# Optimization experiments

Measured on AMD Instinct MI355X. Metric: run time of the kernel, lower is better.

## Reference

```python
import jax, jax.numpy as jnp
import numpy as np

WIN = 11  # hard-coded window size in the original module

def sinusoidal_pe(L, D):
    pos = jnp.arange(L, dtype=jnp.float32)[:, None]
    div = jnp.exp(jnp.arange(0, D, 2, dtype=jnp.float32) * (-np.log(10000.0) / D))
    pe = jnp.zeros((L, D), dtype=jnp.float32)
    pe = pe.at[:, 0::2].set(jnp.sin(pos * div))
    pe = pe.at[:, 1::2].set(jnp.cos(pos * div))
    return pe


def setup_inputs() -> dict:
    key = jax.random.key(0)
    ks = jax.random.split(key, 6)
    B, Lq, Ld, D, V = 16, 30, 1100, 768, 50000
    return {
        "q": jax.random.randint(ks[0], (B, Lq), 0, V),
        "d_pos": jax.random.randint(ks[1], (B, Ld), 0, V),
        "d_neg": jax.random.randint(ks[2], (B, Ld), 0, V),
        "q_mask": jnp.ones((B, Lq, 1), jnp.float32),
        "d_pos_mask": jnp.ones((B, Ld, 1), jnp.float32),
        "d_neg_mask": jnp.ones((B, Ld, 1), jnp.float32),
        "pe_flag": 1,
        "emb_table": jax.random.normal(ks[3], (V, D), jnp.float32) * 0.02,
        "W_lin": jax.random.normal(ks[4], (D, D), jnp.float32) * 0.02,
        "W_out": jax.random.normal(ks[5], (D, D), jnp.float32) * 0.02,
    }


def reference(q, d_pos, d_neg, q_mask, d_pos_mask, d_neg_mask, pe_flag, emb_table, W_lin, W_out):
    B, Lq = q.shape
    Ld = d_pos.shape[1]
    D = emb_table.shape[1]
    H = 12
    Dh = D // H
    W_num = Ld // WIN  # number of 11-token windows

    qe = emb_table[q] * q_mask              # [B,Lq,D]
    dp = emb_table[d_pos]                   # [B,Ld,D]
    dn = emb_table[d_neg]
    if pe_flag:
        pe = sinusoidal_pe(Ld, D)[None]     # [1,Ld,D]
        scale_emb = jnp.sqrt(jnp.float32(D))
        dp = dp * scale_emb + pe            # dropout p=0 -> identity
        dn = dn * scale_emb + pe
    dp = dp * d_pos_mask
    dn = dn * d_neg_mask

    dp = dp.reshape(B, W_num, WIN, D)       # [B,W,11,D]
    dn = dn.reshape(B, W_num, WIN, D)
    qx = jnp.broadcast_to(qe[:, None], (B, W_num, Lq, D))  # expand over windows

    # linear_trans (no bias): y = x @ W_lin.T
    queries = jnp.einsum('bwqd,ed->bwqe', qx, W_lin)
    dp = jnp.einsum('bwkd,ed->bwke', dp, W_lin)
    dn = jnp.einsum('bwkd,ed->bwke', dn, W_lin)

    # faithful replication of torch .view head-split: pure reshape, mixes seq+channel
    def split(x, L):
        return x.reshape(B, W_num, H, L, Dh)

    queries = split(queries, Lq) * (Dh ** -0.5)

    def attend(doc):
        d = split(doc, WIN)                                  # [B,W,H,11,Dh]
        logits = jnp.einsum('bwhqd,bwhkd->bwhqk', queries, d)
        weights = jax.nn.softmax(logits, axis=-1)            # dropout p=0
        ctx = jnp.einsum('bwhqk,bwhkd->bwhqd', weights, d)
        ctx = ctx.reshape(B, W_num, Lq, D)                   # faithful merge (.view)
        return jnp.einsum('bwqd,ed->bwqe', ctx, W_out)

    return attend(dp), attend(dn)
```

## Files before the change

kernel.cpp:

```cpp
#include <hip/hip_runtime.h>
#include <hip/hip_bf16.h>
#include <cstdint>
#include <cstddef>

#define B_    16
#define LQ    30
#define LD    1100
#define DIM   768
#define NH    12
#define DH_   64
#define WINSZ 11
#define WNUM  100
#define NSLOT 32

typedef __attribute__((ext_vector_type(8))) short short8;
typedef __attribute__((ext_vector_type(4))) float f32x4;

__device__ __forceinline__ void gload_lds16(const void* g, void* l) {
  __builtin_amdgcn_global_load_lds(
      (const __attribute__((address_space(1))) void*)g,
      (__attribute__((address_space(3))) void*)l, 16, 0, 0);
}

__global__ __launch_bounds__(256) void wconv_kernel(const float* __restrict__ wa,
    const float* __restrict__ wb, __hip_bfloat16* __restrict__ oa,
    __hip_bfloat16* __restrict__ ob) {
  int i = (blockIdx.x * 256 + threadIdx.x) * 4;
  if (i >= DIM * DIM) return;
  float4 va = *reinterpret_cast<const float4*>(wa + i);
  float4 vb = *reinterpret_cast<const float4*>(wb + i);
  union { __hip_bfloat16 h[4]; uint2 u; } pa, pb;
  pa.h[0] = __float2bfloat16(va.x); pa.h[1] = __float2bfloat16(va.y);
  pa.h[2] = __float2bfloat16(va.z); pa.h[3] = __float2bfloat16(va.w);
  pb.h[0] = __float2bfloat16(vb.x); pb.h[1] = __float2bfloat16(vb.y);
  pb.h[2] = __float2bfloat16(vb.z); pb.h[3] = __float2bfloat16(vb.w);
  *reinterpret_cast<uint2*>(oa + i) = pa.u;
  *reinterpret_cast<uint2*>(ob + i) = pb.u;
}

__global__ __launch_bounds__(256) void pe_kernel(float* __restrict__ pe) {
  int idx = blockIdx.x * 256 + threadIdx.x;
  if (idx >= LD * (DIM / 4)) return;
  int t  = idx / (DIM / 4);
  int c4 = idx % (DIM / 4);
  int i0 = c4 * 2;
  float d0 = expf(-0.023985261387f * (float)i0);
  float d1 = expf(-0.023985261387f * (float)(i0 + 1));
  float s0f, c0f, s1f, c1f;
  sincosf((float)t * d0, &s0f, &c0f);
  sincosf((float)t * d1, &s1f, &c1f);
  *reinterpret_cast<float4*>(pe + (size_t)t * DIM + c4 * 4) =
      make_float4(s0f, c0f, s1f, c1f);
}

__global__ __launch_bounds__(256) void prep_q_kernel(const int* __restrict__ q,
    const float* __restrict__ qmask, const float* __restrict__ emb,
    __hip_bfloat16* __restrict__ Xq) {
  int idx = blockIdx.x * 256 + threadIdx.x;
  if (idx >= B_ * LQ * (DIM / 4)) return;
  int row = idx / (DIM / 4);
  int c4  = idx % (DIM / 4);
  float m = qmask[row] * 0.125f;
  float4 v = *reinterpret_cast<const float4*>(emb + (size_t)q[row] * DIM + c4 * 4);
  union { __hip_bfloat16 h[4]; uint2 u; } o;
  o.h[0] = __float2bfloat16(v.x * m); o.h[1] = __float2bfloat16(v.y * m);
  o.h[2] = __float2bfloat16(v.z * m); o.h[3] = __float2bfloat16(v.w * m);
  *reinterpret_cast<uint2*>(Xq + (size_t)row * DIM + c4 * 4) = o.u;
}

__global__ __launch_bounds__(256) void prep_d_kernel(const int* __restrict__ dpos,
    const int* __restrict__ dneg, const float* __restrict__ dpmask,
    const float* __restrict__ dnmask, const float* __restrict__ emb,
    const int* __restrict__ peflag, const float* __restrict__ pe,
    __hip_bfloat16* __restrict__ X, int s0, int rows) {
  int idx = blockIdx.x * 256 + threadIdx.x;
  if (idx >= rows * (DIM / 4)) return;
  int r  = idx / (DIM / 4);
  int c4 = idx % (DIM / 4);
  int s = s0 + r / LD;
  int t = r % LD;
  int doc = s >> 4, b = s & 15;
  const int*   di = doc ? dneg   : dpos;
  const float* dm = doc ? dnmask : dpmask;
  int grow = b * LD + t;
  float m = dm[grow];
  float4 v = *reinterpret_cast<const float4*>(emb + (size_t)di[grow] * DIM + c4 * 4);
  if (peflag[0]) {
    float4 p = *reinterpret_cast<const float4*>(pe + (size_t)t * DIM + c4 * 4);
    v.x = v.x * 27.712812921102035f + p.x;
    v.y = v.y * 27.712812921102035f + p.y;
    v.z = v.z * 27.712812921102035f + p.z;
    v.w = v.w * 27.712812921102035f + p.w;
  }
  union { __hip_bfloat16 h[4]; uint2 u; } o;
  o.h[0] = __float2bfloat16(v.x * m); o.h[1] = __float2bfloat16(v.y * m);
  o.h[2] = __float2bfloat16(v.z * m); o.h[3] = __float2bfloat16(v.w * m);
  *reinterpret_cast<uint2*>(X + (size_t)r * DIM + c4 * 4) = o.u;
}

template <bool OUT_BF16>
__global__ __launch_bounds__(512, 2) void gemm_mfma(const __hip_bfloat16* __restrict__ A,
    const __hip_bfloat16* __restrict__ Bt, void* __restrict__ Cv,
    int M, int N, int K, int tilesX, int tiles1,
    const __hip_bfloat16* __restrict__ A2, float* __restrict__ C2, int M2) {
  extern __shared__ __hip_bfloat16 smem[];

  const int nwg  = gridDim.x;
  const int orig = blockIdx.x;
  const int q8 = nwg >> 3, r8 = nwg & 7;
  const int xcd = orig & 7, pos = orig >> 3;
  const int wgid = (xcd < r8 ? xcd * (q8 + 1) : r8 * (q8 + 1) + (xcd - r8) * q8) + pos;

  const bool is2 = (wgid >= tiles1);
  const int  w2  = is2 ? (wgid - tiles1) : wgid;
  const int row0 = (w2 / tilesX) * 256;
  const int col0 = (w2 % tilesX) * 256;
  const __hip_bfloat16* Ap = is2 ? A2 : A;
  const int Mloc = is2 ? M2 : M;

  const int tid  = threadIdx.x;
  const int lane = tid & 63;
  const int wave = tid >> 6;
  const int wr = wave >> 2, wc = wave & 3;
  const int lo4 = lane & 15;
  const int hi4 = lane >> 4;

  const int u0 = tid,        r0s = u0 >> 3, x0s = u0 & 7;
  const int u1 = 512 + tid,  r1s = u1 >> 3, x1s = u1 & 7;
  const int soff0 = r0s * K + ((x0s ^ (r0s & 7)) * 8);
  const int soff1 = r1s * K + ((x1s ^ (r1s & 7)) * 8);
  const int wvoff = wave * 512;
  const __hip_bfloat16* gA = Ap + (size_t)row0 * K;
  const __hip_bfloat16* gB = Bt + (size_t)col0 * K;

#define STAGE_HALF(PTR, KOFF, HALF, SLOTBASE)                            \
  gload_lds16((PTR) + (size_t)(HALF) * (128 * 768) + (KOFF) + soff0,    \
              smem + (SLOTBASE) + (HALF) * 8192 + wvoff);               \
  gload_lds16((PTR) + (size_t)(HALF) * (128 * 768) + (KOFF) + soff1,    \
              smem + (SLOTBASE) + (HALF) * 8192 + 4096 + wvoff);

  const int rA = (wr * 128 + lo4) * 64;
  const int rB = (wc * 64  + lo4) * 64;
  const int xk0 = ((0 + hi4) ^ (lo4 & 7)) * 8;
  const int xk1 = ((4 + hi4) ^ (lo4 & 7)) * 8;

#define LDA(S, MM, XK) (*reinterpret_cast<const short8*>(smem + (S) * 16384 + rA + (MM) * 1024 + (XK)))
#define LDB(S, NN, XK) (*reinterpret_cast<const short8*>(smem + 32768 + (S) * 16384 + rB + (NN) * 1024 + (XK)))

  f32x4 acc[8][4] = {};
  short8 bf[4][2];
  short8 xa0, xa1, xa2, xa3;
  short8 ya0, ya1, ya2, ya3;

#define MM4R(MMI, KK, AREG)                                                        \
  acc[MMI][0] = __builtin_amdgcn_mfma_f32_16x16x32_bf16(bf[0][KK], AREG, acc[MMI][0], 0, 0, 0); \
  acc[MMI][1] = __builtin_amdgcn_mfma_f32_16x16x32_bf16(bf[1][KK], AREG, acc[MMI][1], 0, 0, 0); \
  acc[MMI][2] = __builtin_amdgcn_mfma_f32_16x16x32_bf16(bf[2][KK], AREG, acc[MMI][2], 0, 0, 0); \
  acc[MMI][3] = __builtin_amdgcn_mfma_f32_16x16x32_bf16(bf[3][KK], AREG, acc[MMI][3], 0, 0, 0);
#define MFMA4R(MA, MB, R0, R1, R2, R3) \
  MM4R(MA, 0, R0) MM4R(MB, 0, R1) MM4R(MA, 1, R2) MM4R(MB, 1, R3)

#define LDB8(S)                                                          \
  bf[0][0] = LDB(S, 0, xk0); bf[1][0] = LDB(S, 1, xk0);                  \
  bf[2][0] = LDB(S, 2, xk0); bf[3][0] = LDB(S, 3, xk0);                  \
  bf[0][1] = LDB(S, 0, xk1); bf[1][1] = LDB(S, 1, xk1);                  \
  bf[2][1] = LDB(S, 2, xk1); bf[3][1] = LDB(S, 3, xk1);
#define LDA4R(S, MA, MB, R0, R1, R2, R3)                                 \
  R0 = LDA(S, MA, xk0); R1 = LDA(S, MB, xk0);                            \
  R2 = LDA(S, MA, xk1); R3 = LDA(S, MB, xk1);

#define BARR  { __builtin_amdgcn_s_barrier(); __builtin_amdgcn_sched_barrier(0); }
#define VMW(NLIT) asm volatile("s_waitcnt vmcnt(" NLIT ")" ::: "memory");
#define PH_SYNC(NLIT) { asm volatile("s_waitcnt lgkmcnt(" NLIT ")" ::: "memory"); \
                        __builtin_amdgcn_sched_barrier(0);               \
                        __builtin_amdgcn_s_setprio(1); }
#define PH_END  __builtin_amdgcn_s_setprio(0);

  STAGE_HALF(gB, 0,   0, 32768) STAGE_HALF(gB, 0,   1, 32768)
  STAGE_HALF(gA, 0,   0, 0)     STAGE_HALF(gA, 0,   1, 0)
  STAGE_HALF(gB, 64,  0, 49152) STAGE_HALF(gB, 64,  1, 49152)

  for (int it = 0; it < 5; ++it) {
    const int kb = it * 128;
    VMW("4") BARR
    LDB8(0)
    LDA4R(0, 0, 1, xa0, xa1, xa2, xa3)
    LDA4R(0, 2, 3, ya0, ya1, ya2, ya3)
    STAGE_HALF(gA, kb + 64, 0, 16384)
    PH_SYNC("4") MFMA4R(0, 1, xa0, xa1, xa2, xa3) PH_END
    BARR
    LDA4R(0, 4, 5, xa0, xa1, xa2, xa3)
    STAGE_HALF(gA, kb + 64, 1, 16384)
    PH_SYNC("4") MFMA4R(2, 3, ya0, ya1, ya2, ya3) PH_END
    BARR
    LDA4R(0, 6, 7, ya0, ya1, ya2, ya3)
    STAGE_HALF(gB, kb + 128, 0, 32768)
    PH_SYNC("4") MFMA4R(4, 5, xa0, xa1, xa2, xa3) PH_END
    BARR
    STAGE_HALF(gB, kb + 128, 1, 32768)
    PH_SYNC("0") MFMA4R(6, 7, ya0, ya1, ya2, ya3) PH_END
    VMW("4") BARR
    LDB8(1)
    LDA4R(1, 0, 1, xa0, xa1, xa2, xa3)
    LDA4R(1, 2, 3, ya0, ya1, ya2, ya3)
    STAGE_HALF(gA, kb + 128, 0, 0)
    PH_SYNC("4") MFMA4R(0, 1, xa0, xa1, xa2, xa3) PH_END
    BARR
    LDA4R(1, 4, 5, xa0, xa1, xa2, xa3)
    STAGE_HALF(gA, kb + 128, 1, 0)
    PH_SYNC("4") MFMA4R(2, 3, ya0, ya1, ya2, ya3) PH_END
    BARR
    LDA4R(1, 6, 7, ya0, ya1, ya2, ya3)
    STAGE_HALF(gB, kb + 192, 0, 49152)
    PH_SYNC("4") MFMA4R(4, 5, xa0, xa1, xa2, xa3) PH_END
    BARR
    STAGE_HALF(gB, kb + 192, 1, 49152)
    PH_SYNC("0") MFMA4R(6, 7, ya0, ya1, ya2, ya3) PH_END
  }

  VMW("4") BARR
  LDB8(0)
  LDA4R(0, 0, 1, xa0, xa1, xa2, xa3)
  LDA4R(0, 2, 3, ya0, ya1, ya2, ya3)
  STAGE_HALF(gA, 704, 0, 16384)
  PH_SYNC("4") MFMA4R(0, 1, xa0, xa1, xa2, xa3) PH_END
  BARR
  LDA4R(0, 4, 5, xa0, xa1, xa2, xa3)
  STAGE_HALF(gA, 704, 1, 16384)
  PH_SYNC("4") MFMA4R(2, 3, ya0, ya1, ya2, ya3) PH_END
  BARR
  LDA4R(0, 6, 7, ya0, ya1, ya2, ya3)
  PH_SYNC("4") MFMA4R(4, 5, xa0, xa1, xa2, xa3) PH_END
  BARR
  PH_SYNC("0") MFMA4R(6, 7, ya0, ya1, ya2, ya3) PH_END
  VMW("0") BARR
  LDB8(1)
  LDA4R(1, 0, 1, xa0, xa1, xa2, xa3)
  LDA4R(1, 2, 3, ya0, ya1, ya2, ya3)
  PH_SYNC("4") MFMA4R(0, 1, xa0, xa1, xa2, xa3) PH_END
  BARR
  LDA4R(1, 4, 5, xa0, xa1, xa2, xa3)
  PH_SYNC("4") MFMA4R(2, 3, ya0, ya1, ya2, ya3) PH_END
  BARR
  LDA4R(1, 6, 7, ya0, ya1, ya2, ya3)
  PH_SYNC("4") MFMA4R(4, 5, xa0, xa1, xa2, xa3) PH_END
  BARR
  PH_SYNC("0") MFMA4R(6, 7, ya0, ya1, ya2, ya3) PH_END

#undef STAGE_HALF
#undef LDA
#undef LDB
#undef MM4R
#undef MFMA4R
#undef LDB8
#undef LDA4R
#undef BARR
#undef VMW
#undef PH_SYNC
#undef PH_END

#pragma unroll
  for (int m = 0; m < 8; ++m) {
    const int r = row0 + wr * 128 + m * 16 + lo4;
    if (r < Mloc) {
#pragma unroll
      for (int n = 0; n < 4; ++n) {
        const int cb = col0 + wc * 64 + n * 16 + hi4 * 4;
        f32x4 v = acc[m][n];
        if (is2) {
          *reinterpret_cast<f32x4*>(C2 + (size_t)r * N + cb) = v;
        } else if constexpr (OUT_BF16) {
          union { __hip_bfloat16 h[4]; uint2 u; } p;
          p.h[0] = __float2bfloat16(v[0]); p.h[1] = __float2bfloat16(v[1]);
          p.h[2] = __float2bfloat16(v[2]); p.h[3] = __float2bfloat16(v[3]);
          *reinterpret_cast<uint2*>((__hip_bfloat16*)Cv + (size_t)r * N + cb) = p.u;
        } else {
          __builtin_nontemporal_store(
              v, reinterpret_cast<f32x4*>((float*)Cv + (size_t)r * N + cb));
        }
      }
    }
  }
}

__global__ __launch_bounds__(64) void attn_kernel(const float* __restrict__ Qs,
    const __hip_bfloat16* __restrict__ Y, __hip_bfloat16* __restrict__ ctx, int s0) {
  __shared__ alignas(16) __hip_bfloat16 Dk[16][80];
  __shared__ alignas(16) __hip_bfloat16 DlT[64][40];

  const int blk = blockIdx.x;
  const int w  = blk % WNUM;
  const int sl = blk / WNUM;
  const int b  = (s0 + sl) & 15;

  const int lane = threadIdx.x;
  const int lo4 = lane & 15, hi4 = lane >> 4;

  const __hip_bfloat16* Yw = Y + ((size_t)(sl * LD + w * WINSZ)) * DIM;
  const float* Qb = Qs + (size_t)(b * LQ) * DIM;
  __hip_bfloat16* cb = ctx + (size_t)(sl * WNUM + w) * (LQ * DIM);

  for (int h = 0; h < NH; ++h) {
    const uint4* src = reinterpret_cast<const uint4*>(Yw + h * (WINSZ * DH_));
    uint4 r0 = src[lane];
    uint4 r1 = (lane < 24) ? src[64 + lane] : make_uint4(0, 0, 0, 0);
    {
      int k = lane >> 3, d0 = (lane & 7) * 8;
      *reinterpret_cast<uint4*>(&Dk[k][d0]) = r0;
      const __hip_bfloat16* hp = reinterpret_cast<const __hip_bfloat16*>(&r0);
#pragma unroll
      for (int j = 0; j < 8; ++j) DlT[d0 + j][k] = hp[j];
    }
    if (lane < 24) {
      int i = 64 + lane;
      int k = i >> 3, d0 = (i & 7) * 8;
      *reinterpret_cast<uint4*>(&Dk[k][d0]) = r1;
      const __hip_bfloat16* hp = reinterpret_cast<const __hip_bfloat16*>(&r1);
#pragma unroll
      for (int j = 0; j < 8; ++j) DlT[d0 + j][k] = hp[j];
    }
    asm volatile("s_waitcnt lgkmcnt(0)" ::: "memory");

    f32x4 sT[2] = {};
#pragma unroll
    for (int half = 0; half < 2; ++half) {
      short8 dfrag = *reinterpret_cast<const short8*>(&Dk[lo4][half * 32 + hi4 * 8]);
#pragma unroll
      for (int qt = 0; qt < 2; ++qt) {
        const float* qp = Qb + (size_t)(qt * 16 + lo4) * DIM + h * 64 + half * 32 + hi4 * 8;
        float4 qa = *reinterpret_cast<const float4*>(qp);
        float4 qc = *reinterpret_cast<const float4*>(qp + 4);
        union { __hip_bfloat16 hh[8]; short8 s; } qf;
        qf.hh[0] = __float2bfloat16(qa.x); qf.hh[1] = __float2bfloat16(qa.y);
        qf.hh[2] = __float2bfloat16(qa.z); qf.hh[3] = __float2bfloat16(qa.w);
        qf.hh[4] = __float2bfloat16(qc.x); qf.hh[5] = __float2bfloat16(qc.y);
        qf.hh[6] = __float2bfloat16(qc.z); qf.hh[7] = __float2bfloat16(qc.w);
        sT[qt] = __builtin_amdgcn_mfma_f32_16x16x32_bf16(dfrag, qf.s, sT[qt], 0, 0, 0);
      }
    }

    uint pk[2][2];
#pragma unroll
    for (int qt = 0; qt < 2; ++qt) {
      float mx = -1e30f;
#pragma unroll
      for (int j = 0; j < 4; ++j) {
        int k = hi4 * 4 + j;
        if (k < WINSZ) mx = fmaxf(mx, sT[qt][j]);
      }
      mx = fmaxf(mx, __shfl_xor(mx, 16));
      mx = fmaxf(mx, __shfl_xor(mx, 32));
      float p[4]; float sum = 0.f;
#pragma unroll
      for (int j = 0; j < 4; ++j) {
        int k = hi4 * 4 + j;
        p[j] = (k < WINSZ) ? expf(sT[qt][j] - mx) : 0.f;
        sum += p[j];
      }
      sum += __shfl_xor(sum, 16);
      sum += __shfl_xor(sum, 32);
      float iv = 1.f / sum;
      union { __hip_bfloat16 h[2]; uint u; } u01, u23;
      u01.h[0] = __float2bfloat16(p[0] * iv); u01.h[1] = __float2bfloat16(p[1] * iv);
      u23.h[0] = __float2bfloat16(p[2] * iv); u23.h[1] = __float2bfloat16(p[3] * iv);
      pk[qt][0] = u01.u; pk[qt][1] = u23.u;
    }

    short8 pfrag[2];
    {
      int g0 = ((hi4 * 2) & 3) * 16 + lo4;
      int g1 = ((hi4 * 2 + 1) & 3) * 16 + lo4;
#pragma unroll
      for (int qt = 0; qt < 2; ++qt) {
        uint w0 = __builtin_amdgcn_ds_bpermute(g0 * 4, pk[qt][0]);
        uint w1 = __builtin_amdgcn_ds_bpermute(g0 * 4, pk[qt][1]);
        uint w2 = __builtin_amdgcn_ds_bpermute(g1 * 4, pk[qt][0]);
        uint w3 = __builtin_amdgcn_ds_bpermute(g1 * 4, pk[qt][1]);
        if (hi4 >= 2) { w0 = 0; w1 = 0; w2 = 0; w3 = 0; }
        union { uint u[4]; short8 s; } asm8;
        asm8.u[0] = w0; asm8.u[1] = w1; asm8.u[2] = w2; asm8.u[3] = w3;
        pfrag[qt] = asm8.s;
      }
    }

    f32x4 oacc[4][2] = {};
#pragma unroll
    for (int dt = 0; dt < 4; ++dt) {
      short8 dtf = *reinterpret_cast<const short8*>(&DlT[dt * 16 + lo4][hi4 * 8]);
#pragma unroll
      for (int qt = 0; qt < 2; ++qt)
        oacc[dt][qt] = __builtin_amdgcn_mfma_f32_16x16x32_bf16(dtf, pfrag[qt], oacc[dt][qt], 0, 0, 0);
    }

#pragma unroll
    for (int qt = 0; qt < 2; ++qt) {
      int q = qt * 16 + lo4;
      if (q < LQ) {
#pragma unroll
        for (int dt = 0; dt < 4; ++dt) {
          f32x4 v = oacc[dt][qt];
          union { __hip_bfloat16 h[4]; uint2 u; } p;
          p.h[0] = __float2bfloat16(v[0]); p.h[1] = __float2bfloat16(v[1]);
          p.h[2] = __float2bfloat16(v[2]); p.h[3] = __float2bfloat16(v[3]);
          *reinterpret_cast<uint2*>(cb + h * (LQ * DH_) + q * DH_ + dt * 16 + hi4 * 4) = p.u;
        }
      }
    }
    asm volatile("s_waitcnt lgkmcnt(0)" ::: "memory");
  }
}

extern "C" void kernel_launch(void* const* d_in, const int* in_sizes, int n_in,
                              void* d_out, int out_size, void* d_ws, size_t ws_size,
                              hipStream_t stream) {
  const int*   q      = (const int*)d_in[0];
  const int*   dpos   = (const int*)d_in[1];
  const int*   dneg   = (const int*)d_in[2];
  const float* qmask  = (const float*)d_in[3];
  const float* dpmask = (const float*)d_in[4];
  const float* dnmask = (const float*)d_in[5];
  const int*   peflag = (const int*)d_in[6];
  const float* emb    = (const float*)d_in[7];
  const float* Wlin   = (const float*)d_in[8];
  const float* Wout   = (const float*)d_in[9];
  float* out = (float*)d_out;

  (void)hipFuncSetAttribute(reinterpret_cast<const void*>(&gemm_mfma<false>),
                            hipFuncAttributeMaxDynamicSharedMemorySize, 131072);
  (void)hipFuncSetAttribute(reinterpret_cast<const void*>(&gemm_mfma<true>),
                            hipFuncAttributeMaxDynamicSharedMemorySize, 131072);

  char* ws = (char*)d_ws;
  size_t off = 0;
  auto alloc = [&](size_t bytes) -> char* {
    char* p = ws + off; off += (bytes + 255) & ~(size_t)255; return p;
  };
  __hip_bfloat16* Xq   = (__hip_bfloat16*)alloc((size_t)512 * DIM * 2);
  float*          Qsc  = (float*)         alloc((size_t)512 * DIM * 4);
  __hip_bfloat16* Wl16 = (__hip_bfloat16*)alloc((size_t)DIM * DIM * 2);
  __hip_bfloat16* Wo16 = (__hip_bfloat16*)alloc((size_t)DIM * DIM * 2);
  float*          PE   = (float*)         alloc((size_t)LD * DIM * 4);

  int SC = NSLOT;
  while (SC > 1) {
    size_t need = off
        + ((size_t)SC * LD + 256) * DIM * 2 * 2
        + ((size_t)SC * WNUM * LQ + 256) * DIM * 2 + (1u << 20);
    if (need <= ws_size) break;
    SC >>= 1;
  }
  __hip_bfloat16* X   = (__hip_bfloat16*)alloc(((size_t)SC * LD + 256) * DIM * 2);
  __hip_bfloat16* Y   = (__hip_bfloat16*)alloc(((size_t)SC * LD + 256) * DIM * 2);
  __hip_bfloat16* ctx = (__hip_bfloat16*)alloc(((size_t)SC * WNUM * LQ + 256) * DIM * 2);

  wconv_kernel<<<(DIM * DIM / 4 + 255) / 256, 256, 0, stream>>>(Wlin, Wout, Wl16, Wo16);
  pe_kernel<<<(LD * (DIM / 4) + 255) / 256, 256, 0, stream>>>(PE);
  prep_q_kernel<<<(B_ * LQ * (DIM / 4) + 255) / 256, 256, 0, stream>>>(q, qmask, emb, Xq);

  const int tilesX = DIM / 256;
  const int qTiles = tilesX * ((B_ * LQ + 255) / 256);

  for (int s0 = 0; s0 < NSLOT; s0 += SC) {
    const int rowsX = SC * LD;
    const int rowsC = SC * WNUM * LQ;
    prep_d_kernel<<<(rowsX * (DIM / 4) + 255) / 256, 256, 0, stream>>>(
        dpos, dneg, dpmask, dnmask, emb, peflag, PE, X, s0, rowsX);
    {
      int tiles1 = tilesX * ((rowsX + 255) / 256);
      int t2 = (s0 == 0) ? qTiles : 0;
      gemm_mfma<true><<<tiles1 + t2, 512, 131072, stream>>>(
          X, Wl16, Y, rowsX, DIM, DIM, tilesX, tiles1, Xq, Qsc, B_ * LQ);
    }
    attn_kernel<<<SC * WNUM, 64, 0, stream>>>(Qsc, Y, ctx, s0);
    {
      int tiles1 = tilesX * ((rowsC + 255) / 256);
      gemm_mfma<false><<<tiles1, 512, 131072, stream>>>(
          ctx, Wo16, out + (size_t)s0 * WNUM * LQ * DIM, rowsC, DIM, DIM,
          tilesX, tiles1, nullptr, nullptr, 0);
    }
  }
}
```

Before: 334.6 us.

## Merge prologue kernels, widen prep_d to 8 elements, raise MFMA priority

Folds the weight-conversion, positional-encoding and query-prep kernels into one launch that dispatches on block index, cutting two kernel launches. prep_d now handles 8 columns per thread with 16-byte bf16 stores instead of 4 columns with 8-byte stores, halving the thread count. The attention kernel raises wave priority around its PV MFMA loop. Launch overhead savings are small, and the wider per-thread work lowers memory-level parallelism per thread in the gather.

```diff
diff --git a/kernel.cpp b/kernel.cpp
--- a/kernel.cpp
+++ b/kernel.cpp
@@ -22,50 +22,54 @@
       (__attribute__((address_space(3))) void*)l, 16, 0, 0);
 }
 
-__global__ __launch_bounds__(256) void wconv_kernel(const float* __restrict__ wa,
-    const float* __restrict__ wb, __hip_bfloat16* __restrict__ oa,
-    __hip_bfloat16* __restrict__ ob) {
-  int i = (blockIdx.x * 256 + threadIdx.x) * 4;
-  if (i >= DIM * DIM) return;
-  float4 va = *reinterpret_cast<const float4*>(wa + i);
-  float4 vb = *reinterpret_cast<const float4*>(wb + i);
-  union { __hip_bfloat16 h[4]; uint2 u; } pa, pb;
-  pa.h[0] = __float2bfloat16(va.x); pa.h[1] = __float2bfloat16(va.y);
-  pa.h[2] = __float2bfloat16(va.z); pa.h[3] = __float2bfloat16(va.w);
-  pb.h[0] = __float2bfloat16(vb.x); pb.h[1] = __float2bfloat16(vb.y);
-  pb.h[2] = __float2bfloat16(vb.z); pb.h[3] = __float2bfloat16(vb.w);
-  *reinterpret_cast<uint2*>(oa + i) = pa.u;
-  *reinterpret_cast<uint2*>(ob + i) = pb.u;
-}
-
-__global__ __launch_bounds__(256) void pe_kernel(float* __restrict__ pe) {
-  int idx = blockIdx.x * 256 + threadIdx.x;
-  if (idx >= LD * (DIM / 4)) return;
-  int t  = idx / (DIM / 4);
-  int c4 = idx % (DIM / 4);
-  int i0 = c4 * 2;
-  float d0 = expf(-0.023985261387f * (float)i0);
-  float d1 = expf(-0.023985261387f * (float)(i0 + 1));
-  float s0f, c0f, s1f, c1f;
-  sincosf((float)t * d0, &s0f, &c0f);
-  sincosf((float)t * d1, &s1f, &c1f);
-  *reinterpret_cast<float4*>(pe + (size_t)t * DIM + c4 * 4) =
-      make_float4(s0f, c0f, s1f, c1f);
-}
-
-__global__ __launch_bounds__(256) void prep_q_kernel(const int* __restrict__ q,
-    const float* __restrict__ qmask, const float* __restrict__ emb,
-    __hip_bfloat16* __restrict__ Xq) {
-  int idx = blockIdx.x * 256 + threadIdx.x;
-  if (idx >= B_ * LQ * (DIM / 4)) return;
-  int row = idx / (DIM / 4);
-  int c4  = idx % (DIM / 4);
-  float m = qmask[row] * 0.125f;
-  float4 v = *reinterpret_cast<const float4*>(emb + (size_t)q[row] * DIM + c4 * 4);
-  union { __hip_bfloat16 h[4]; uint2 u; } o;
-  o.h[0] = __float2bfloat16(v.x * m); o.h[1] = __float2bfloat16(v.y * m);
-  o.h[2] = __float2bfloat16(v.z * m); o.h[3] = __float2bfloat16(v.w * m);
-  *reinterpret_cast<uint2*>(Xq + (size_t)row * DIM + c4 * 4) = o.u;
+#define WCONV_B ((DIM * DIM / 4 + 255) / 256)
+#define PE_B    ((LD * (DIM / 4) + 255) / 256)
+#define PQ_B    ((B_ * LQ * (DIM / 4) + 255) / 256)
+
+__global__ __launch_bounds__(256) void prologue_kernel(
+    const float* __restrict__ wa, const float* __restrict__ wb,
+    __hip_bfloat16* __restrict__ oa, __hip_bfloat16* __restrict__ ob,
+    float* __restrict__ pe,
+    const int* __restrict__ q, const float* __restrict__ qmask,
+    const float* __restrict__ emb, __hip_bfloat16* __restrict__ Xq) {
+  int bx = blockIdx.x;
+  if (bx < WCONV_B) {
+    int i = (bx * 256 + threadIdx.x) * 4;
+    if (i >= DIM * DIM) return;
+    float4 va = *reinterpret_cast<const float4*>(wa + i);
+    float4 vb = *reinterpret_cast<const float4*>(wb + i);
+    union { __hip_bfloat16 h[4]; uint2 u; } pa, pb;
+    pa.h[0] = __float2bfloat16(va.x); pa.h[1] = __float2bfloat16(va.y);
+    pa.h[2] = __float2bfloat16(va.z); pa.h[3] = __float2bfloat16(va.w);
+    pb.h[0] = __float2bfloat16(vb.x); pb.h[1] = __float2bfloat16(vb.y);
+    pb.h[2] = __float2bfloat16(vb.z); pb.h[3] = __float2bfloat16(vb.w);
+    *reinterpret_cast<uint2*>(oa + i) = pa.u;
+    *reinterpret_cast<uint2*>(ob + i) = pb.u;
+  } else if (bx < WCONV_B + PE_B) {
+    int idx = (bx - WCONV_B) * 256 + threadIdx.x;
+    if (idx >= LD * (DIM / 4)) return;
+    int t  = idx / (DIM / 4);
+    int c4 = idx % (DIM / 4);
+    int i0 = c4 * 2;
+    float d0 = expf(-0.023985261387f * (float)i0);
+    float d1 = expf(-0.023985261387f * (float)(i0 + 1));
+    float s0f, c0f, s1f, c1f;
+    sincosf((float)t * d0, &s0f, &c0f);
+    sincosf((float)t * d1, &s1f, &c1f);
+    *reinterpret_cast<float4*>(pe + (size_t)t * DIM + c4 * 4) =
+        make_float4(s0f, c0f, s1f, c1f);
+  } else {
+    int idx = (bx - WCONV_B - PE_B) * 256 + threadIdx.x;
+    if (idx >= B_ * LQ * (DIM / 4)) return;
+    int row = idx / (DIM / 4);
+    int c4  = idx % (DIM / 4);
+    float m = qmask[row] * 0.125f;
+    float4 v = *reinterpret_cast<const float4*>(emb + (size_t)q[row] * DIM + c4 * 4);
+    union { __hip_bfloat16 h[4]; uint2 u; } o;
+    o.h[0] = __float2bfloat16(v.x * m); o.h[1] = __float2bfloat16(v.y * m);
+    o.h[2] = __float2bfloat16(v.z * m); o.h[3] = __float2bfloat16(v.w * m);
+    *reinterpret_cast<uint2*>(Xq + (size_t)row * DIM + c4 * 4) = o.u;
+  }
 }
 
 __global__ __launch_bounds__(256) void prep_d_kernel(const int* __restrict__ dpos,
@@ -74,9 +78,10 @@
     const int* __restrict__ peflag, const float* __restrict__ pe,
     __hip_bfloat16* __restrict__ X, int s0, int rows) {
   int idx = blockIdx.x * 256 + threadIdx.x;
-  if (idx >= rows * (DIM / 4)) return;
-  int r  = idx / (DIM / 4);
-  int c4 = idx % (DIM / 4);
+  if (idx >= rows * (DIM / 8)) return;
+  int r  = idx / (DIM / 8);
+  int c8 = idx % (DIM / 8);
+  int col = c8 * 8;
   int s = s0 + r / LD;
   int t = r % LD;
   int doc = s >> 4, b = s & 15;
@@ -84,18 +89,28 @@
   const float* dm = doc ? dnmask : dpmask;
   int grow = b * LD + t;
   float m = dm[grow];
-  float4 v = *reinterpret_cast<const float4*>(emb + (size_t)di[grow] * DIM + c4 * 4);
+  const float* ep = emb + (size_t)di[grow] * DIM + col;
+  float4 v0 = *reinterpret_cast<const float4*>(ep);
+  float4 v1 = *reinterpret_cast<const float4*>(ep + 4);
   if (peflag[0]) {
-    float4 p = *reinterpret_cast<const float4*>(pe + (size_t)t * DIM + c4 * 4);
-    v.x = v.x * 27.712812921102035f + p.x;
-    v.y = v.y * 27.712812921102035f + p.y;
-    v.z = v.z * 27.712812921102035f + p.z;
-    v.w = v.w * 27.712812921102035f + p.w;
-  }
-  union { __hip_bfloat16 h[4]; uint2 u; } o;
-  o.h[0] = __float2bfloat16(v.x * m); o.h[1] = __float2bfloat16(v.y * m);
-  o.h[2] = __float2bfloat16(v.z * m); o.h[3] = __float2bfloat16(v.w * m);
-  *reinterpret_cast<uint2*>(X + (size_t)r * DIM + c4 * 4) = o.u;
+    const float* pp = pe + (size_t)t * DIM + col;
+    float4 p0 = *reinterpret_cast<const float4*>(pp);
+    float4 p1 = *reinterpret_cast<const float4*>(pp + 4);
+    v0.x = v0.x * 27.712812921102035f + p0.x;
+    v0.y = v0.y * 27.712812921102035f + p0.y;
+    v0.z = v0.z * 27.712812921102035f + p0.z;
+    v0.w = v0.w * 27.712812921102035f + p0.w;
+    v1.x = v1.x * 27.712812921102035f + p1.x;
+    v1.y = v1.y * 27.712812921102035f + p1.y;
+    v1.z = v1.z * 27.712812921102035f + p1.z;
+    v1.w = v1.w * 27.712812921102035f + p1.w;
+  }
+  union { __hip_bfloat16 h[8]; uint4 u; } o;
+  o.h[0] = __float2bfloat16(v0.x * m); o.h[1] = __float2bfloat16(v0.y * m);
+  o.h[2] = __float2bfloat16(v0.z * m); o.h[3] = __float2bfloat16(v0.w * m);
+  o.h[4] = __float2bfloat16(v1.x * m); o.h[5] = __float2bfloat16(v1.y * m);
+  o.h[6] = __float2bfloat16(v1.z * m); o.h[7] = __float2bfloat16(v1.w * m);
+  *reinterpret_cast<uint4*>(X + (size_t)r * DIM + col) = o.u;
 }
 
 template <bool OUT_BF16>
@@ -384,6 +399,7 @@
     }
 
     f32x4 oacc[4][2] = {};
+    __builtin_amdgcn_s_setprio(1);
 #pragma unroll
     for (int dt = 0; dt < 4; ++dt) {
       short8 dtf = *reinterpret_cast<const short8*>(&DlT[dt * 16 + lo4][hi4 * 8]);
@@ -391,6 +407,7 @@
       for (int qt = 0; qt < 2; ++qt)
         oacc[dt][qt] = __builtin_amdgcn_mfma_f32_16x16x32_bf16(dtf, pfrag[qt], oacc[dt][qt], 0, 0, 0);
     }
+    __builtin_amdgcn_s_setprio(0);
 
 #pragma unroll
     for (int qt = 0; qt < 2; ++qt) {
@@ -453,9 +470,8 @@
   __hip_bfloat16* Y   = (__hip_bfloat16*)alloc(((size_t)SC * LD + 256) * DIM * 2);
   __hip_bfloat16* ctx = (__hip_bfloat16*)alloc(((size_t)SC * WNUM * LQ + 256) * DIM * 2);
 
-  wconv_kernel<<<(DIM * DIM / 4 + 255) / 256, 256, 0, stream>>>(Wlin, Wout, Wl16, Wo16);
-  pe_kernel<<<(LD * (DIM / 4) + 255) / 256, 256, 0, stream>>>(PE);
-  prep_q_kernel<<<(B_ * LQ * (DIM / 4) + 255) / 256, 256, 0, stream>>>(q, qmask, emb, Xq);
+  prologue_kernel<<<WCONV_B + PE_B + PQ_B, 256, 0, stream>>>(
+      Wlin, Wout, Wl16, Wo16, PE, q, qmask, emb, Xq);
 
   const int tilesX = DIM / 256;
   const int qTiles = tilesX * ((B_ * LQ + 255) / 256);
@@ -463,7 +479,7 @@
   for (int s0 = 0; s0 < NSLOT; s0 += SC) {
     const int rowsX = SC * LD;
     const int rowsC = SC * WNUM * LQ;
-    prep_d_kernel<<<(rowsX * (DIM / 4) + 255) / 256, 256, 0, stream>>>(
+    prep_d_kernel<<<(rowsX * (DIM / 8) + 255) / 256, 256, 0, stream>>>(
         dpos, dneg, dpmask, dnmask, emb, peflag, PE, X, s0, rowsX);
     {
       int tiles1 = tilesX * ((rowsX + 255) / 256);
```

Result: faster. 327.8 us, median of 2 (-2.0%).
